# Kernel optimization log

Hardware: AMD Instinct MI355X
Metric: run time of the kernel (lower is better)

## Reference

```python
import jax, jax.numpy as jnp
import numpy as np

# DeepSeek V4 MLA sparse attention dims
T = 512            # query tokens
H = 64             # attention heads (SUPPORTED_HEAD_COUNTS)
KV_LORA = 512      # kv_lora_rank (value dim = latent nope part)
ROPE = 64          # qk_rope_head_dim
D = KV_LORA + ROPE # 576 = head_dim (matches alignment=576 in cache spec)
N_KV = 8192        # cached compressed-KV tokens
TOPK = 1024        # top-k selected tokens per query
SCALE = 1.0 / np.sqrt(D).astype(np.float32)


def setup_inputs() -> dict:
    key = jax.random.key(0)
    k1, k2, k3, k4 = jax.random.split(key, 4)
    q = jax.random.normal(k1, (T, H, D), dtype=jnp.float32)
    kv = jax.random.normal(k2, (N_KV, D), dtype=jnp.float32)   # compressed KV latent cache (1 kv head)
    topk_idx = jax.random.randint(k3, (T, TOPK), 0, N_KV, dtype=jnp.int32)
    sink = jax.random.normal(k4, (H,), dtype=jnp.float32)       # per-head attention sink logit
    return {"q": q, "kv": kv, "topk_idx": topk_idx, "sink": sink}


def reference(q, kv, topk_idx, sink):
    # Sparse MLA: each query token attends only to its top-k latent cache slots.
    valid = topk_idx >= 0                       # invalid slots marked negative
    idx = jnp.maximum(topk_idx, 0)
    g = kv[idx]                                  # [T, K, D] gathered latents
    # scores over gathered subset: [T, H, K]
    scores = jnp.einsum('thd,tkd->thk', q, g) * SCALE
    scores = jnp.where(valid[:, None, :], scores, -jnp.inf)
    # sink-aware softmax: sink acts as an extra logit with zero value
    m = jnp.maximum(jnp.max(scores, axis=-1), sink[None, :])   # [T, H]
    p = jnp.exp(scores - m[..., None])                          # [T, H, K]
    denom = jnp.sum(p, axis=-1) + jnp.exp(sink[None, :] - m)    # [T, H]
    # value = nope part (first KV_LORA dims) of latent -> output [T, H, KV_LORA]
    out = jnp.einsum('thk,tkv->thv', p, g[..., :KV_LORA]) / denom[..., None]
    return out
```

## Files before the change

### kernel.cpp

```cpp
#include <hip/hip_runtime.h>
#include <hip/hip_bf16.h>

#define T_TOK 512
#define NH    64
#define HD    576
#define DVAL  512
#define NKV   8192
#define TOPK  1024
#define KT    32
#define NITER (TOPK / KT)
#define KSTEPS (HD / 32)
#define SCALE 0.041666666666666664f
#define LOG2E 1.4426950408889634f
#define QSCL  (SCALE * LOG2E)
#define MFIX  8.0f
#define MB    (MFIX * LOG2E)

typedef __attribute__((ext_vector_type(4))) float f32x4;
typedef __attribute__((ext_vector_type(8))) _Float16 half8;
typedef __attribute__((ext_vector_type(4))) unsigned short us4;
typedef __attribute__((ext_vector_type(8))) unsigned short us8;
typedef __attribute__((ext_vector_type(4))) int i32x4;

__device__ __forceinline__ unsigned short f2h(float x) {
    _Float16 h = (_Float16)x;
    return __builtin_bit_cast(unsigned short, h);
}

__device__ __forceinline__ float fexp2(float x) {
#if __has_builtin(__builtin_amdgcn_exp2f)
    return __builtin_amdgcn_exp2f(x);
#else
    return __expf(x * 0.6931471805599453f);
#endif
}

template<int CTRL>
__device__ __forceinline__ float dppmv(float x) {
    int r = __builtin_amdgcn_update_dpp(0, __builtin_bit_cast(int, x), CTRL, 0xF, 0xF, true);
    return __builtin_bit_cast(float, r);
}
__device__ __forceinline__ float red16sum(float x) {
    x += dppmv<0xB1>(x);
    x += dppmv<0x4E>(x);
    x += dppmv<0x141>(x);
    x += dppmv<0x140>(x);
    return x;
}

#define TICK_BARRIER() do {                                   \
    asm volatile("s_waitcnt lgkmcnt(0)" ::: "memory");        \
    __builtin_amdgcn_s_barrier();                             \
    asm volatile("" ::: "memory");                            \
} while (0)

__global__ void cvt_kv_f16(const float* __restrict__ kv, unsigned short* __restrict__ kvb) {
    int i = blockIdx.x * 256 + threadIdx.x;
    const f32x4* src = (const f32x4*)kv + (size_t)i * 2;
    f32x4 a = src[0];
    f32x4 b = src[1];
    us8 w;
    w[0]=f2h(a[0]); w[1]=f2h(a[1]); w[2]=f2h(a[2]); w[3]=f2h(a[3]);
    w[4]=f2h(b[0]); w[5]=f2h(b[1]); w[6]=f2h(b[2]); w[7]=f2h(b[3]);
    ((us8*)kvb)[i] = w;
}

#define G_LD  584
#define P_LD  40
#define GT_IDX(row,key) (((((row) << 5) | (key))) ^ ((((row) >> 2) & 7) << 3))

struct StageRegs { us8 v[4]; us4 rope; };

__device__ __forceinline__ void stage_load(
    const unsigned short* __restrict__ kvb, const int* __restrict__ tkrow,
    int it, int w8, int kg, int lm, int quad, int l16, StageRegs& R)
{
    const int* ip = tkrow + it * KT + kg * 4;
    i32x4 r4 = *(const i32x4*)ip;
    int d0 = w8 * 64 + lm * 8;
    #pragma unroll
    for (int j = 0; j < 4; j++) {
        int r = r4[j] < 0 ? 0 : r4[j];
        R.v[j] = *(const us8*)(kvb + (size_t)r * HD + d0);
    }
    int kr = tkrow[it * KT + w8 * 4 + quad];
    if (kr < 0) kr = 0;
    R.rope = *(const us4*)(kvb + (size_t)kr * HD + 512 + l16 * 4);
}

__device__ __forceinline__ void stage_write(
    int w8, int kg, int lm, int quad, int l16, const StageRegs& R,
    unsigned short (*gp)[G_LD], unsigned short* gtp)
{
    int d0 = w8 * 64 + lm * 8;
    #pragma unroll
    for (int j = 0; j < 4; j++)
        *(us8*)&gp[kg * 4 + j][d0] = R.v[j];
    #pragma unroll
    for (int e = 0; e < 8; e++) {
        us4 wv;
        wv[0] = R.v[0][e]; wv[1] = R.v[1][e]; wv[2] = R.v[2][e]; wv[3] = R.v[3][e];
        *(us4*)&gtp[GT_IDX(d0 + e, kg * 4)] = wv;
    }
    *(us4*)&gp[w8 * 4 + quad][512 + l16 * 4] = R.rope;
}

__device__ __forceinline__ void pv_tick(
    int tau, const unsigned short* __restrict__ kvb, const int* __restrict__ tkrow,
    int w8, int kg, int lm, int quad, int l16, int col0,
    StageRegs& Lset, StageRegs& Wset,
    unsigned short (*g2p)[G_LD], unsigned short* gtp,
    const unsigned short (*pb)[P_LD],
    f32x4 (&acc)[4][4])
{
    if (tau + 2 < NITER)
        stage_load(kvb, tkrow, tau + 2, w8, kg, lm, quad, l16, Lset);

    half8 pa[4];
    #pragma unroll
    for (int mt = 0; mt < 4; mt++)
        pa[mt] = *(const half8*)&pb[mt * 16 + l16][quad * 8];

    __builtin_amdgcn_s_setprio(1);
    #pragma unroll
    for (int nt = 0; nt < 4; nt++) {
        half8 vb = *(const half8*)&gtp[GT_IDX(col0 + nt * 16 + l16, quad * 8)];
        #pragma unroll
        for (int mt = 0; mt < 4; mt++)
            acc[mt][nt] = __builtin_amdgcn_mfma_f32_16x16x32_f16(pa[mt], vb, acc[mt][nt], 0, 0, 0);
    }
    __builtin_amdgcn_s_setprio(0);

    asm volatile("s_waitcnt lgkmcnt(0)" ::: "memory");
    if (tau + 1 < NITER)
        stage_write(w8, kg, lm, quad, l16, Wset, g2p, gtp);
}

__global__ __launch_bounds__(768, 3) void mla_sparse_kernel(
    const float* __restrict__ q, const int* __restrict__ topk,
    const float* __restrict__ sink, const unsigned short* __restrict__ kvb,
    float* __restrict__ out)
{
    __shared__ unsigned short g2[2][KT][G_LD];
    __shared__ unsigned short gtb[2][DVAL * KT];
    __shared__ unsigned short pbuf[2][NH][P_LD];
    __shared__ float lrunL[NH];

    const int t    = blockIdx.x;
    const int tid  = threadIdx.x;
    const int lane = tid & 63;
    const int quad = lane >> 4;
    const int l16  = lane & 15;
    const int wave = __builtin_amdgcn_readfirstlane(tid >> 6);
    const int* tkrow = topk + (size_t)t * TOPK;

    if (wave < 4) {
        const int w  = wave;
        const int qo = quad * 8;
        half8 qf[KSTEPS];
        {
            const float* qrow = q + ((size_t)t * NH + (w * 16 + l16)) * HD;
            #pragma unroll
            for (int ks = 0; ks < KSTEPS; ks++) {
                int d0 = ks * 32 + qo;
                f32x4 a = *(const f32x4*)(qrow + d0);
                f32x4 b = *(const f32x4*)(qrow + d0 + 4);
                half8 h;
                h[0]=(_Float16)(a[0]*QSCL); h[1]=(_Float16)(a[1]*QSCL);
                h[2]=(_Float16)(a[2]*QSCL); h[3]=(_Float16)(a[3]*QSCL);
                h[4]=(_Float16)(b[0]*QSCL); h[5]=(_Float16)(b[1]*QSCL);
                h[6]=(_Float16)(b[2]*QSCL); h[7]=(_Float16)(b[3]*QSCL);
                qf[ks] = h;
            }
        }
        unsigned mb0 = 0, mb1 = 0;
        #pragma unroll 4
        for (int kk = 0; kk < NITER; kk++) {
            mb0 |= (tkrow[kk * KT + l16]      < 0) ? (1u << kk) : 0u;
            mb1 |= (tkrow[kk * KT + 16 + l16] < 0) ? (1u << kk) : 0u;
        }
        f32x4 sk = *(const f32x4*)(sink + w * 16 + quad * 4);
        float l_part[4];
        #pragma unroll
        for (int r = 0; r < 4; r++)
            l_part[r] = (l16 == 0) ? fexp2(sk[r] * LOG2E - MB) : 0.0f;
        const int hb = w * 16 + quad * 4;

        __syncthreads();

        for (int k = 0; k <= NITER; k++) {
            if (k < NITER) {
                const int par = k & 1;
                const unsigned short (*gp)[G_LD] = g2[par];
                f32x4 zero = {0.f, 0.f, 0.f, 0.f};
                f32x4 mbase = {-MB, -MB, -MB, -MB};
                f32x4 s0a = mbase, s0b = zero, s1a = mbase, s1b = zero;
                __builtin_amdgcn_s_setprio(1);
                #pragma unroll
                for (int ks = 0; ks < KSTEPS; ks += 2) {
                    half8 b0 = *(const half8*)&gp[l16][ks * 32 + qo];
                    half8 b1 = *(const half8*)&gp[16 + l16][ks * 32 + qo];
                    s0a = __builtin_amdgcn_mfma_f32_16x16x32_f16(qf[ks], b0, s0a, 0, 0, 0);
                    s1a = __builtin_amdgcn_mfma_f32_16x16x32_f16(qf[ks], b1, s1a, 0, 0, 0);
                    half8 c0 = *(const half8*)&gp[l16][ks * 32 + 32 + qo];
                    half8 c1 = *(const half8*)&gp[16 + l16][ks * 32 + 32 + qo];
                    s0b = __builtin_amdgcn_mfma_f32_16x16x32_f16(qf[ks+1], c0, s0b, 0, 0, 0);
                    s1b = __builtin_amdgcn_mfma_f32_16x16x32_f16(qf[ks+1], c1, s1b, 0, 0, 0);
                }
                __builtin_amdgcn_s_setprio(0);
                f32x4 s0 = s0a + s0b, s1 = s1a + s1b;
                const bool bad0 = (mb0 >> k) & 1;
                const bool bad1 = (mb1 >> k) & 1;
                const float NEG = -__builtin_inff();
                #pragma unroll
                for (int r = 0; r < 4; r++) {
                    float v0 = bad0 ? NEG : s0[r];
                    float v1 = bad1 ? NEG : s1[r];
                    float p0 = fexp2(v0);
                    float p1 = fexp2(v1);
                    l_part[r] += p0 + p1;
                    pbuf[par][hb + r][l16]      = f2h(p0);
                    pbuf[par][hb + r][16 + l16] = f2h(p1);
                }
            }
            TICK_BARRIER();
        }
        #pragma unroll
        for (int r = 0; r < 4; r++) l_part[r] = red16sum(l_part[r]);
        if (l16 == 0) {
            f32x4 l4; l4[0]=l_part[0]; l4[1]=l_part[1]; l4[2]=l_part[2]; l4[3]=l_part[3];
            *(f32x4*)&lrunL[hb] = l4;
        }
        __syncthreads();
    } else {
        const int w8   = wave - 4;
        const int col0 = w8 * 64;
        const int kg   = lane >> 3;
        const int lm   = lane & 7;
        f32x4 acc[4][4];
        f32x4 zero = {0.f, 0.f, 0.f, 0.f};
        #pragma unroll
        for (int mt = 0; mt < 4; mt++)
            #pragma unroll
            for (int nt = 0; nt < 4; nt++) acc[mt][nt] = zero;

        StageRegs A, B;
        stage_load(kvb, tkrow, 0, w8, kg, lm, quad, l16, A);
        stage_write(w8, kg, lm, quad, l16, A, g2[0], gtb[0]);
        stage_load(kvb, tkrow, 1, w8, kg, lm, quad, l16, B);
        __syncthreads();

        stage_load(kvb, tkrow, 2, w8, kg, lm, quad, l16, A);
        stage_write(w8, kg, lm, quad, l16, B, g2[1], gtb[1]);
        TICK_BARRIER();

        for (int k = 1; k < NITER; k += 2) {
            pv_tick(k, kvb, tkrow, w8, kg, lm, quad, l16, col0,
                    B, A, g2[0], gtb[0], pbuf[0], acc);
            TICK_BARRIER();
            pv_tick(k + 1, kvb, tkrow, w8, kg, lm, quad, l16, col0,
                    A, B, g2[1], gtb[1], pbuf[1], acc);
            TICK_BARRIER();
        }
        __syncthreads();

        #pragma unroll
        for (int mt = 0; mt < 4; mt++) {
            f32x4 lv = *(const f32x4*)&lrunL[mt * 16 + quad * 4];
            f32x4 li;
            li[0] = 1.0f / lv[0]; li[1] = 1.0f / lv[1];
            li[2] = 1.0f / lv[2]; li[3] = 1.0f / lv[3];
            #pragma unroll
            for (int nt = 0; nt < 4; nt++) {
                int vcol = col0 + nt * 16 + l16;
                f32x4 r = acc[mt][nt] * li;
                #pragma unroll
                for (int rr = 0; rr < 4; rr++) {
                    int head = mt * 16 + quad * 4 + rr;
                    out[((size_t)t * NH + head) * DVAL + vcol] = r[rr];
                }
            }
        }
    }
}

extern "C" void kernel_launch(void* const* d_in, const int* in_sizes, int n_in,
                              void* d_out, int out_size, void* d_ws, size_t ws_size,
                              hipStream_t stream) {
    const float* q    = (const float*)d_in[0];
    const float* kv   = (const float*)d_in[1];
    const int*   topk = (const int*)d_in[2];
    const float* sink = (const float*)d_in[3];
    float* out = (float*)d_out;
    unsigned short* kvb = (unsigned short*)d_ws;

    cvt_kv_f16<<<NKV * HD / (256 * 8), 256, 0, stream>>>(kv, kvb);
    mla_sparse_kernel<<<T_TOK, 768, 0, stream>>>(q, topk, sink, kvb, out);
}
```

Baseline: 255.5 us.

## Load rope slice directly from global in score waves instead of LDS staging

The PV producer waves no longer stage the 64-wide rope part of each gathered KV row into shared memory. Instead the score waves fetch their rope fragments straight from global memory each iteration and feed them to the final MFMAs. This shrinks the LDS row stride from 584 to 520 and drops the precomputed invalid-index bitmasks, which are now derived from the per-iteration index loads. The trade-off is added global-load latency on the score path, which sits on the critical QK path with no prefetch.

```diff
diff --git a/kernel.cpp b/kernel.cpp
--- a/kernel.cpp
+++ b/kernel.cpp
@@ -9,7 +9,7 @@
 #define TOPK  1024
 #define KT    32
 #define NITER (TOPK / KT)
-#define KSTEPS (HD / 32)
+#define KSTEPS_L 16
 #define SCALE 0.041666666666666664f
 #define LOG2E 1.4426950408889634f
 #define QSCL  (SCALE * LOG2E)
@@ -65,15 +65,15 @@
     ((us8*)kvb)[i] = w;
 }
 
-#define G_LD  584
+#define G_LD  520
 #define P_LD  40
 #define GT_IDX(row,key) (((((row) << 5) | (key))) ^ ((((row) >> 2) & 7) << 3))
 
-struct StageRegs { us8 v[4]; us4 rope; };
+struct StageRegs { us8 v[4]; };
 
 __device__ __forceinline__ void stage_load(
     const unsigned short* __restrict__ kvb, const int* __restrict__ tkrow,
-    int it, int w8, int kg, int lm, int quad, int l16, StageRegs& R)
+    int it, int w8, int kg, int lm, StageRegs& R)
 {
     const int* ip = tkrow + it * KT + kg * 4;
     i32x4 r4 = *(const i32x4*)ip;
@@ -83,13 +83,10 @@
         int r = r4[j] < 0 ? 0 : r4[j];
         R.v[j] = *(const us8*)(kvb + (size_t)r * HD + d0);
     }
-    int kr = tkrow[it * KT + w8 * 4 + quad];
-    if (kr < 0) kr = 0;
-    R.rope = *(const us4*)(kvb + (size_t)kr * HD + 512 + l16 * 4);
 }
 
 __device__ __forceinline__ void stage_write(
-    int w8, int kg, int lm, int quad, int l16, const StageRegs& R,
+    int w8, int kg, int lm, const StageRegs& R,
     unsigned short (*gp)[G_LD], unsigned short* gtp)
 {
     int d0 = w8 * 64 + lm * 8;
@@ -102,7 +99,6 @@
         wv[0] = R.v[0][e]; wv[1] = R.v[1][e]; wv[2] = R.v[2][e]; wv[3] = R.v[3][e];
         *(us4*)&gtp[GT_IDX(d0 + e, kg * 4)] = wv;
     }
-    *(us4*)&gp[w8 * 4 + quad][512 + l16 * 4] = R.rope;
 }
 
 __device__ __forceinline__ void pv_tick(
@@ -114,7 +110,7 @@
     f32x4 (&acc)[4][4])
 {
     if (tau + 2 < NITER)
-        stage_load(kvb, tkrow, tau + 2, w8, kg, lm, quad, l16, Lset);
+        stage_load(kvb, tkrow, tau + 2, w8, kg, lm, Lset);
 
     half8 pa[4];
     #pragma unroll
@@ -133,7 +129,7 @@
 
     asm volatile("s_waitcnt lgkmcnt(0)" ::: "memory");
     if (tau + 1 < NITER)
-        stage_write(w8, kg, lm, quad, l16, Wset, g2p, gtp);
+        stage_write(w8, kg, lm, Wset, g2p, gtp);
 }
 
 __global__ __launch_bounds__(768, 3) void mla_sparse_kernel(
@@ -157,11 +153,11 @@
     if (wave < 4) {
         const int w  = wave;
         const int qo = quad * 8;
-        half8 qf[KSTEPS];
+        half8 qf[18];
         {
             const float* qrow = q + ((size_t)t * NH + (w * 16 + l16)) * HD;
             #pragma unroll
-            for (int ks = 0; ks < KSTEPS; ks++) {
+            for (int ks = 0; ks < 18; ks++) {
                 int d0 = ks * 32 + qo;
                 f32x4 a = *(const f32x4*)(qrow + d0);
                 f32x4 b = *(const f32x4*)(qrow + d0 + 4);
@@ -173,12 +169,6 @@
                 qf[ks] = h;
             }
         }
-        unsigned mb0 = 0, mb1 = 0;
-        #pragma unroll 4
-        for (int kk = 0; kk < NITER; kk++) {
-            mb0 |= (tkrow[kk * KT + l16]      < 0) ? (1u << kk) : 0u;
-            mb1 |= (tkrow[kk * KT + 16 + l16] < 0) ? (1u << kk) : 0u;
-        }
         f32x4 sk = *(const f32x4*)(sink + w * 16 + quad * 4);
         float l_part[4];
         #pragma unroll
@@ -192,12 +182,23 @@
             if (k < NITER) {
                 const int par = k & 1;
                 const unsigned short (*gp)[G_LD] = g2[par];
+                int raw0 = tkrow[k * KT + l16];
+                int raw1 = tkrow[k * KT + 16 + l16];
+                int ra = raw0 < 0 ? 0 : raw0;
+                int rb = raw1 < 0 ? 0 : raw1;
+                const unsigned short* rpA = kvb + (size_t)ra * HD + 512 + qo;
+                const unsigned short* rpB = kvb + (size_t)rb * HD + 512 + qo;
+                half8 r0a = *(const half8*)(rpA);
+                half8 r0b = *(const half8*)(rpB);
+                half8 r1a = *(const half8*)(rpA + 32);
+                half8 r1b = *(const half8*)(rpB + 32);
+
                 f32x4 zero = {0.f, 0.f, 0.f, 0.f};
                 f32x4 mbase = {-MB, -MB, -MB, -MB};
                 f32x4 s0a = mbase, s0b = zero, s1a = mbase, s1b = zero;
                 __builtin_amdgcn_s_setprio(1);
                 #pragma unroll
-                for (int ks = 0; ks < KSTEPS; ks += 2) {
+                for (int ks = 0; ks < KSTEPS_L; ks += 2) {
                     half8 b0 = *(const half8*)&gp[l16][ks * 32 + qo];
                     half8 b1 = *(const half8*)&gp[16 + l16][ks * 32 + qo];
                     s0a = __builtin_amdgcn_mfma_f32_16x16x32_f16(qf[ks], b0, s0a, 0, 0, 0);
@@ -207,10 +208,14 @@
                     s0b = __builtin_amdgcn_mfma_f32_16x16x32_f16(qf[ks+1], c0, s0b, 0, 0, 0);
                     s1b = __builtin_amdgcn_mfma_f32_16x16x32_f16(qf[ks+1], c1, s1b, 0, 0, 0);
                 }
+                s0a = __builtin_amdgcn_mfma_f32_16x16x32_f16(qf[16], r0a, s0a, 0, 0, 0);
+                s1a = __builtin_amdgcn_mfma_f32_16x16x32_f16(qf[16], r0b, s1a, 0, 0, 0);
+                s0b = __builtin_amdgcn_mfma_f32_16x16x32_f16(qf[17], r1a, s0b, 0, 0, 0);
+                s1b = __builtin_amdgcn_mfma_f32_16x16x32_f16(qf[17], r1b, s1b, 0, 0, 0);
                 __builtin_amdgcn_s_setprio(0);
                 f32x4 s0 = s0a + s0b, s1 = s1a + s1b;
-                const bool bad0 = (mb0 >> k) & 1;
-                const bool bad1 = (mb1 >> k) & 1;
+                const bool bad0 = raw0 < 0;
+                const bool bad1 = raw1 < 0;
                 const float NEG = -__builtin_inff();
                 #pragma unroll
                 for (int r = 0; r < 4; r++) {
@@ -245,13 +250,13 @@
             for (int nt = 0; nt < 4; nt++) acc[mt][nt] = zero;
 
         StageRegs A, B;
-        stage_load(kvb, tkrow, 0, w8, kg, lm, quad, l16, A);
-        stage_write(w8, kg, lm, quad, l16, A, g2[0], gtb[0]);
-        stage_load(kvb, tkrow, 1, w8, kg, lm, quad, l16, B);
+        stage_load(kvb, tkrow, 0, w8, kg, lm, A);
+        stage_write(w8, kg, lm, A, g2[0], gtb[0]);
+        stage_load(kvb, tkrow, 1, w8, kg, lm, B);
         __syncthreads();
 
-        stage_load(kvb, tkrow, 2, w8, kg, lm, quad, l16, A);
-        stage_write(w8, kg, lm, quad, l16, B, g2[1], gtb[1]);
+        stage_load(kvb, tkrow, 2, w8, kg, lm, A);
+        stage_write(w8, kg, lm, B, g2[1], gtb[1]);
         TICK_BARRIER();
 
         for (int k = 1; k < NITER; k += 2) {
```

New measurement: 263.1 us. 1.03x slower.

## Load gathered KV rows directly into LDS via global_load_lds with swizzled layout

Applied to the files above, without the earlier changes.

The row-major gathered KV tile and its rope part are now fetched with direct global-to-LDS loads (global_load_lds) into a new XOR-swizzled 512-wide layout plus a separate rope buffer, instead of going through registers and ds_write. The QK waves index the swizzled layout. The register path stays only for the transposed copy used by PV, and explicit vmcnt waits order the asynchronous loads before the barriers. This is meant to cut VGPR traffic and LDS write instructions on the producer waves, but it loads the nope part twice from global memory and depends on hand-counted vmcnt values being correct.

```diff
diff --git a/kernel.cpp b/kernel.cpp
--- a/kernel.cpp
+++ b/kernel.cpp
@@ -9,7 +9,6 @@
 #define TOPK  1024
 #define KT    32
 #define NITER (TOPK / KT)
-#define KSTEPS (HD / 32)
 #define SCALE 0.041666666666666664f
 #define LOG2E 1.4426950408889634f
 #define QSCL  (SCALE * LOG2E)
@@ -53,6 +52,16 @@
     __builtin_amdgcn_s_barrier();                             \
     asm volatile("" ::: "memory");                            \
 } while (0)
+
+#if __has_builtin(__builtin_amdgcn_global_load_lds)
+#define HAVE_GLOAD 1
+#define GLOAD16(src, ldsbase)                                              \
+    __builtin_amdgcn_global_load_lds(                                      \
+        (const __attribute__((address_space(1))) void*)(src),              \
+        (__attribute__((address_space(3))) void*)(ldsbase), 16, 0, 0)
+#else
+#define HAVE_GLOAD 0
+#endif
 
 __global__ void cvt_kv_f16(const float* __restrict__ kv, unsigned short* __restrict__ kvb) {
     int i = blockIdx.x * 256 + threadIdx.x;
@@ -65,15 +74,51 @@
     ((us8*)kvb)[i] = w;
 }
 
-#define G_LD  584
 #define P_LD  40
 #define GT_IDX(row,key) (((((row) << 5) | (key))) ^ ((((row) >> 2) & 7) << 3))
 
-struct StageRegs { us8 v[4]; us4 rope; };
+struct StageRegs { us8 v[4]; };
+
+__device__ __forceinline__ void stage_gload(
+    const unsigned short* __restrict__ kvb, const int* __restrict__ tkrow,
+    int it, int w8, int lane, unsigned short* g2d, unsigned short* roped)
+{
+#if HAVE_GLOAD
+    #pragma unroll
+    for (int j = 0; j < 4; j++) {
+        int key = w8 * 4 + j;
+        int row = tkrow[it * KT + key]; row = row < 0 ? 0 : row;
+        int chunk = lane ^ (key & 7);
+        GLOAD16(kvb + (size_t)row * HD + chunk * 8, g2d + key * 512);
+    }
+    if (w8 < 4) {
+        int key = w8 * 8 + (lane >> 3);
+        int row = tkrow[it * KT + key]; row = row < 0 ? 0 : row;
+        int chunk = (lane & 7) ^ (key & 7);
+        GLOAD16(kvb + (size_t)row * HD + 512 + chunk * 8, roped + w8 * 512);
+    }
+#else
+    #pragma unroll
+    for (int j = 0; j < 4; j++) {
+        int key = w8 * 4 + j;
+        int row = tkrow[it * KT + key]; row = row < 0 ? 0 : row;
+        int chunk = lane ^ (key & 7);
+        *(us8*)&g2d[key * 512 + lane * 8] =
+            *(const us8*)(kvb + (size_t)row * HD + chunk * 8);
+    }
+    if (w8 < 4) {
+        int key = w8 * 8 + (lane >> 3);
+        int row = tkrow[it * KT + key]; row = row < 0 ? 0 : row;
+        int chunk = (lane & 7) ^ (key & 7);
+        *(us8*)&roped[w8 * 512 + lane * 8] =
+            *(const us8*)(kvb + (size_t)row * HD + 512 + chunk * 8);
+    }
+#endif
+}
 
 __device__ __forceinline__ void stage_load(
     const unsigned short* __restrict__ kvb, const int* __restrict__ tkrow,
-    int it, int w8, int kg, int lm, int quad, int l16, StageRegs& R)
+    int it, int w8, int kg, int lm, StageRegs& R)
 {
     const int* ip = tkrow + it * KT + kg * 4;
     i32x4 r4 = *(const i32x4*)ip;
@@ -83,38 +128,34 @@
         int r = r4[j] < 0 ? 0 : r4[j];
         R.v[j] = *(const us8*)(kvb + (size_t)r * HD + d0);
     }
-    int kr = tkrow[it * KT + w8 * 4 + quad];
-    if (kr < 0) kr = 0;
-    R.rope = *(const us4*)(kvb + (size_t)kr * HD + 512 + l16 * 4);
-}
-
-__device__ __forceinline__ void stage_write(
-    int w8, int kg, int lm, int quad, int l16, const StageRegs& R,
-    unsigned short (*gp)[G_LD], unsigned short* gtp)
+}
+
+__device__ __forceinline__ void stage_write_gt(
+    int w8, int kg, int lm, const StageRegs& R, unsigned short* gtp)
 {
     int d0 = w8 * 64 + lm * 8;
-    #pragma unroll
-    for (int j = 0; j < 4; j++)
-        *(us8*)&gp[kg * 4 + j][d0] = R.v[j];
     #pragma unroll
     for (int e = 0; e < 8; e++) {
         us4 wv;
         wv[0] = R.v[0][e]; wv[1] = R.v[1][e]; wv[2] = R.v[2][e]; wv[3] = R.v[3][e];
         *(us4*)&gtp[GT_IDX(d0 + e, kg * 4)] = wv;
     }
-    *(us4*)&gp[w8 * 4 + quad][512 + l16 * 4] = R.rope;
 }
 
 __device__ __forceinline__ void pv_tick(
     int tau, const unsigned short* __restrict__ kvb, const int* __restrict__ tkrow,
-    int w8, int kg, int lm, int quad, int l16, int col0,
+    int w8, int kg, int lm, int quad, int l16, int lane, int col0,
     StageRegs& Lset, StageRegs& Wset,
-    unsigned short (*g2p)[G_LD], unsigned short* gtp,
+    unsigned short* g2d_next, unsigned short* roped_next, unsigned short* gtp,
     const unsigned short (*pb)[P_LD],
     f32x4 (&acc)[4][4])
 {
-    if (tau + 2 < NITER)
-        stage_load(kvb, tkrow, tau + 2, w8, kg, lm, quad, l16, Lset);
+    const bool do_next  = (tau + 1 < NITER);
+    const bool do_load2 = (tau + 2 < NITER);
+    if (do_next)
+        stage_gload(kvb, tkrow, tau + 1, w8, lane, g2d_next, roped_next);
+    if (do_load2)
+        stage_load(kvb, tkrow, tau + 2, w8, kg, lm, Lset);
 
     half8 pa[4];
     #pragma unroll
@@ -132,8 +173,11 @@
     __builtin_amdgcn_s_setprio(0);
 
     asm volatile("s_waitcnt lgkmcnt(0)" ::: "memory");
-    if (tau + 1 < NITER)
-        stage_write(w8, kg, lm, quad, l16, Wset, g2p, gtp);
+    if (do_next) {
+        stage_write_gt(w8, kg, lm, Wset, gtp);
+        if (do_load2) asm volatile("s_waitcnt vmcnt(4)" ::: "memory");
+        else          asm volatile("s_waitcnt vmcnt(0)" ::: "memory");
+    }
 }
 
 __global__ __launch_bounds__(768, 3) void mla_sparse_kernel(
@@ -141,27 +185,28 @@
     const float* __restrict__ sink, const unsigned short* __restrict__ kvb,
     float* __restrict__ out)
 {
-    __shared__ unsigned short g2[2][KT][G_LD];
+    __shared__ unsigned short g2s[2][KT * 512];
+    __shared__ unsigned short ropes[2][KT * 64];
     __shared__ unsigned short gtb[2][DVAL * KT];
     __shared__ unsigned short pbuf[2][NH][P_LD];
     __shared__ float lrunL[NH];
 
-    const int t    = blockIdx.x;
     const int tid  = threadIdx.x;
     const int lane = tid & 63;
     const int quad = lane >> 4;
     const int l16  = lane & 15;
     const int wave = __builtin_amdgcn_readfirstlane(tid >> 6);
+    const int t    = blockIdx.x;
     const int* tkrow = topk + (size_t)t * TOPK;
 
     if (wave < 4) {
         const int w  = wave;
         const int qo = quad * 8;
-        half8 qf[KSTEPS];
+        half8 qf[18];
         {
             const float* qrow = q + ((size_t)t * NH + (w * 16 + l16)) * HD;
             #pragma unroll
-            for (int ks = 0; ks < KSTEPS; ks++) {
+            for (int ks = 0; ks < 18; ks++) {
                 int d0 = ks * 32 + qo;
                 f32x4 a = *(const f32x4*)(qrow + d0);
                 f32x4 b = *(const f32x4*)(qrow + d0 + 4);
@@ -179,6 +224,11 @@
             mb0 |= (tkrow[kk * KT + l16]      < 0) ? (1u << kk) : 0u;
             mb1 |= (tkrow[kk * KT + 16 + l16] < 0) ? (1u << kk) : 0u;
         }
+        const int k7    = l16 & 7;
+        const int sidx0 = l16 * 512 + ((quad ^ k7) << 3);
+        const int sidx1 = l16 * 512 + (((4 + quad) ^ k7) << 3);
+        const int ridx0 = l16 * 64 + ((quad ^ k7) << 3);
+        const int ridx1 = l16 * 64 + (((4 + quad) ^ k7) << 3);
         f32x4 sk = *(const f32x4*)(sink + w * 16 + quad * 4);
         float l_part[4];
         #pragma unroll
@@ -191,21 +241,33 @@
         for (int k = 0; k <= NITER; k++) {
             if (k < NITER) {
                 const int par = k & 1;
-                const unsigned short (*gp)[G_LD] = g2[par];
+                const unsigned short* gp = g2s[par];
+                const unsigned short* rp = ropes[par];
                 f32x4 zero = {0.f, 0.f, 0.f, 0.f};
                 f32x4 mbase = {-MB, -MB, -MB, -MB};
                 f32x4 s0a = mbase, s0b = zero, s1a = mbase, s1b = zero;
                 __builtin_amdgcn_s_setprio(1);
                 #pragma unroll
-                for (int ks = 0; ks < KSTEPS; ks += 2) {
-                    half8 b0 = *(const half8*)&gp[l16][ks * 32 + qo];
-                    half8 b1 = *(const half8*)&gp[16 + l16][ks * 32 + qo];
+                for (int ks = 0; ks < 16; ks += 2) {
+                    int o = (ks >> 1) * 64;
+                    half8 b0 = *(const half8*)&gp[sidx0 + o];
+                    half8 b1 = *(const half8*)&gp[sidx0 + 8192 + o];
                     s0a = __builtin_amdgcn_mfma_f32_16x16x32_f16(qf[ks], b0, s0a, 0, 0, 0);
                     s1a = __builtin_amdgcn_mfma_f32_16x16x32_f16(qf[ks], b1, s1a, 0, 0, 0);
-                    half8 c0 = *(const half8*)&gp[l16][ks * 32 + 32 + qo];
-                    half8 c1 = *(const half8*)&gp[16 + l16][ks * 32 + 32 + qo];
+                    half8 c0 = *(const half8*)&gp[sidx1 + o];
+                    half8 c1 = *(const half8*)&gp[sidx1 + 8192 + o];
                     s0b = __builtin_amdgcn_mfma_f32_16x16x32_f16(qf[ks+1], c0, s0b, 0, 0, 0);
                     s1b = __builtin_amdgcn_mfma_f32_16x16x32_f16(qf[ks+1], c1, s1b, 0, 0, 0);
+                }
+                {
+                    half8 r0 = *(const half8*)&rp[ridx0];
+                    half8 r1 = *(const half8*)&rp[ridx0 + 1024];
+                    s0a = __builtin_amdgcn_mfma_f32_16x16x32_f16(qf[16], r0, s0a, 0, 0, 0);
+                    s1a = __builtin_amdgcn_mfma_f32_16x16x32_f16(qf[16], r1, s1a, 0, 0, 0);
+                    half8 r2 = *(const half8*)&rp[ridx1];
+                    half8 r3 = *(const half8*)&rp[ridx1 + 1024];
+                    s0b = __builtin_amdgcn_mfma_f32_16x16x32_f16(qf[17], r2, s0b, 0, 0, 0);
+                    s1b = __builtin_amdgcn_mfma_f32_16x16x32_f16(qf[17], r3, s1b, 0, 0, 0);
                 }
                 __builtin_amdgcn_s_setprio(0);
                 f32x4 s0 = s0a + s0b, s1 = s1a + s1b;
@@ -245,21 +307,26 @@
             for (int nt = 0; nt < 4; nt++) acc[mt][nt] = zero;
 
         StageRegs A, B;
-        stage_load(kvb, tkrow, 0, w8, kg, lm, quad, l16, A);
-        stage_write(w8, kg, lm, quad, l16, A, g2[0], gtb[0]);
-        stage_load(kvb, tkrow, 1, w8, kg, lm, quad, l16, B);
+        stage_gload(kvb, tkrow, 0, w8, lane, g2s[0], ropes[0]);
+        stage_load(kvb, tkrow, 0, w8, kg, lm, A);
+        stage_write_gt(w8, kg, lm, A, gtb[0]);
+        stage_load(kvb, tkrow, 1, w8, kg, lm, B);
+        asm volatile("s_waitcnt vmcnt(4)" ::: "memory");
         __syncthreads();
 
-        stage_load(kvb, tkrow, 2, w8, kg, lm, quad, l16, A);
-        stage_write(w8, kg, lm, quad, l16, B, g2[1], gtb[1]);
+        stage_gload(kvb, tkrow, 1, w8, lane, g2s[1], ropes[1]);
+        stage_load(kvb, tkrow, 2, w8, kg, lm, A);
+        asm volatile("s_waitcnt lgkmcnt(0)" ::: "memory");
+        stage_write_gt(w8, kg, lm, B, gtb[1]);
+        asm volatile("s_waitcnt vmcnt(4)" ::: "memory");
         TICK_BARRIER();
 
         for (int k = 1; k < NITER; k += 2) {
-            pv_tick(k, kvb, tkrow, w8, kg, lm, quad, l16, col0,
-                    B, A, g2[0], gtb[0], pbuf[0], acc);
+            pv_tick(k, kvb, tkrow, w8, kg, lm, quad, l16, lane, col0,
+                    B, A, g2s[0], ropes[0], gtb[0], pbuf[0], acc);
             TICK_BARRIER();
-            pv_tick(k + 1, kvb, tkrow, w8, kg, lm, quad, l16, col0,
-                    A, B, g2[1], gtb[1], pbuf[1], acc);
+            pv_tick(k + 1, kvb, tkrow, w8, kg, lm, quad, l16, lane, col0,
+                    A, B, g2s[1], ropes[1], gtb[1], pbuf[1], acc);
             TICK_BARRIER();
         }
         __syncthreads();
```

Measured after the change: 258.0 us. About the same (+1.0%).

## Use ds_read_b64_tr_b16 transpose reads instead of separate transposed LDS copy

Applied to the files above, without the earlier changes.

Replaces the dual LDS layout (row-major gathered KV plus a separately written transposed copy for the PV matmul) with a single subtiled layout of 4-key groups. The PV waves now read V operands with the hardware transposing LDS load ds_read_b64_tr_b16, and the QK waves index into the new subtile layout. This removes the per-element scatter of the transposed buffer and halves LDS footprint, at the cost of inline asm, a full lgkmcnt wait before the MFMAs, and new bank-conflict behavior from the subtile stride.

```diff
diff --git a/kernel.cpp b/kernel.cpp
--- a/kernel.cpp
+++ b/kernel.cpp
@@ -9,12 +9,14 @@
 #define TOPK  1024
 #define KT    32
 #define NITER (TOPK / KT)
-#define KSTEPS (HD / 32)
+#define KSTEPS 18
 #define SCALE 0.041666666666666664f
 #define LOG2E 1.4426950408889634f
 #define QSCL  (SCALE * LOG2E)
 #define MFIX  8.0f
 #define MB    (MFIX * LOG2E)
+#define SKG   2312
+#define P_LD  36
 
 typedef __attribute__((ext_vector_type(4))) float f32x4;
 typedef __attribute__((ext_vector_type(8))) _Float16 half8;
@@ -65,10 +67,6 @@
     ((us8*)kvb)[i] = w;
 }
 
-#define G_LD  584
-#define P_LD  40
-#define GT_IDX(row,key) (((((row) << 5) | (key))) ^ ((((row) >> 2) & 7) << 3))
-
 struct StageRegs { us8 v[4]; us4 rope; };
 
 __device__ __forceinline__ void stage_load(
@@ -88,28 +86,24 @@
     R.rope = *(const us4*)(kvb + (size_t)kr * HD + 512 + l16 * 4);
 }
 
-__device__ __forceinline__ void stage_write(
+__device__ __forceinline__ void stage_write_sub(
     int w8, int kg, int lm, int quad, int l16, const StageRegs& R,
-    unsigned short (*gp)[G_LD], unsigned short* gtp)
+    unsigned short* g2d)
 {
-    int d0 = w8 * 64 + lm * 8;
+    int chunk = w8 * 4 + (lm >> 1);
+    int off   = (lm & 1) * 8;
+    int base  = kg * SKG + chunk * 64 + off;
     #pragma unroll
     for (int j = 0; j < 4; j++)
-        *(us8*)&gp[kg * 4 + j][d0] = R.v[j];
-    #pragma unroll
-    for (int e = 0; e < 8; e++) {
-        us4 wv;
-        wv[0] = R.v[0][e]; wv[1] = R.v[1][e]; wv[2] = R.v[2][e]; wv[3] = R.v[3][e];
-        *(us4*)&gtp[GT_IDX(d0 + e, kg * 4)] = wv;
-    }
-    *(us4*)&gp[w8 * 4 + quad][512 + l16 * 4] = R.rope;
+        *(us8*)&g2d[base + j * 16] = R.v[j];
+    *(us4*)&g2d[w8 * SKG + (32 + (l16 >> 2)) * 64 + quad * 16 + (l16 & 3) * 4] = R.rope;
 }
 
 __device__ __forceinline__ void pv_tick(
     int tau, const unsigned short* __restrict__ kvb, const int* __restrict__ tkrow,
     int w8, int kg, int lm, int quad, int l16, int col0,
     StageRegs& Lset, StageRegs& Wset,
-    unsigned short (*g2p)[G_LD], unsigned short* gtp,
+    unsigned short* g2_w, const unsigned short* g2_r,
     const unsigned short (*pb)[P_LD],
     f32x4 (&acc)[4][4])
 {
@@ -121,19 +115,33 @@
     for (int mt = 0; mt < 4; mt++)
         pa[mt] = *(const half8*)&pb[mt * 16 + l16][quad * 8];
 
+    us4 t0[4], t1[4];
+    const unsigned gbase = (unsigned)(size_t)g2_r;
+    #pragma unroll
+    for (int nt = 0; nt < 4; nt++) {
+        unsigned a0 = gbase + 2u * ((quad * 2 + 0) * SKG + (w8 * 4 + nt) * 64) + 8u * l16;
+        unsigned a1 = gbase + 2u * ((quad * 2 + 1) * SKG + (w8 * 4 + nt) * 64) + 8u * l16;
+        asm volatile("ds_read_b64_tr_b16 %0, %1" : "=v"(t0[nt]) : "v"(a0));
+        asm volatile("ds_read_b64_tr_b16 %0, %1" : "=v"(t1[nt]) : "v"(a1));
+    }
+    asm volatile("s_waitcnt lgkmcnt(0)" ::: "memory");
+    __builtin_amdgcn_sched_barrier(0);
+
     __builtin_amdgcn_s_setprio(1);
     #pragma unroll
     for (int nt = 0; nt < 4; nt++) {
-        half8 vb = *(const half8*)&gtp[GT_IDX(col0 + nt * 16 + l16, quad * 8)];
+        us8 wv;
+        wv[0]=t0[nt][0]; wv[1]=t0[nt][1]; wv[2]=t0[nt][2]; wv[3]=t0[nt][3];
+        wv[4]=t1[nt][0]; wv[5]=t1[nt][1]; wv[6]=t1[nt][2]; wv[7]=t1[nt][3];
+        half8 vb = __builtin_bit_cast(half8, wv);
         #pragma unroll
         for (int mt = 0; mt < 4; mt++)
             acc[mt][nt] = __builtin_amdgcn_mfma_f32_16x16x32_f16(pa[mt], vb, acc[mt][nt], 0, 0, 0);
     }
     __builtin_amdgcn_s_setprio(0);
 
-    asm volatile("s_waitcnt lgkmcnt(0)" ::: "memory");
     if (tau + 1 < NITER)
-        stage_write(w8, kg, lm, quad, l16, Wset, g2p, gtp);
+        stage_write_sub(w8, kg, lm, quad, l16, Wset, g2_w);
 }
 
 __global__ __launch_bounds__(768, 3) void mla_sparse_kernel(
@@ -141,17 +149,16 @@
     const float* __restrict__ sink, const unsigned short* __restrict__ kvb,
     float* __restrict__ out)
 {
-    __shared__ unsigned short g2[2][KT][G_LD];
-    __shared__ unsigned short gtb[2][DVAL * KT];
+    __shared__ unsigned short g2sub[2][8 * SKG];
     __shared__ unsigned short pbuf[2][NH][P_LD];
     __shared__ float lrunL[NH];
 
-    const int t    = blockIdx.x;
     const int tid  = threadIdx.x;
     const int lane = tid & 63;
     const int quad = lane >> 4;
     const int l16  = lane & 15;
     const int wave = __builtin_amdgcn_readfirstlane(tid >> 6);
+    const int t    = blockIdx.x;
     const int* tkrow = topk + (size_t)t * TOPK;
 
     if (wave < 4) {
@@ -179,6 +186,8 @@
             mb0 |= (tkrow[kk * KT + l16]      < 0) ? (1u << kk) : 0u;
             mb1 |= (tkrow[kk * KT + 16 + l16] < 0) ? (1u << kk) : 0u;
         }
+        const int baseA = (l16 >> 2) * SKG + (l16 & 3) * 16 + (quad >> 1) * 64 + (quad & 1) * 8;
+        const int baseB = baseA + 4 * SKG;
         f32x4 sk = *(const f32x4*)(sink + w * 16 + quad * 4);
         float l_part[4];
         #pragma unroll
@@ -191,19 +200,19 @@
         for (int k = 0; k <= NITER; k++) {
             if (k < NITER) {
                 const int par = k & 1;
-                const unsigned short (*gp)[G_LD] = g2[par];
+                const unsigned short* gp = g2sub[par];
                 f32x4 zero = {0.f, 0.f, 0.f, 0.f};
                 f32x4 mbase = {-MB, -MB, -MB, -MB};
                 f32x4 s0a = mbase, s0b = zero, s1a = mbase, s1b = zero;
                 __builtin_amdgcn_s_setprio(1);
                 #pragma unroll
                 for (int ks = 0; ks < KSTEPS; ks += 2) {
-                    half8 b0 = *(const half8*)&gp[l16][ks * 32 + qo];
-                    half8 b1 = *(const half8*)&gp[16 + l16][ks * 32 + qo];
+                    half8 b0 = *(const half8*)&gp[baseA + ks * 128];
+                    half8 b1 = *(const half8*)&gp[baseB + ks * 128];
                     s0a = __builtin_amdgcn_mfma_f32_16x16x32_f16(qf[ks], b0, s0a, 0, 0, 0);
                     s1a = __builtin_amdgcn_mfma_f32_16x16x32_f16(qf[ks], b1, s1a, 0, 0, 0);
-                    half8 c0 = *(const half8*)&gp[l16][ks * 32 + 32 + qo];
-                    half8 c1 = *(const half8*)&gp[16 + l16][ks * 32 + 32 + qo];
+                    half8 c0 = *(const half8*)&gp[baseA + (ks + 1) * 128];
+                    half8 c1 = *(const half8*)&gp[baseB + (ks + 1) * 128];
                     s0b = __builtin_amdgcn_mfma_f32_16x16x32_f16(qf[ks+1], c0, s0b, 0, 0, 0);
                     s1b = __builtin_amdgcn_mfma_f32_16x16x32_f16(qf[ks+1], c1, s1b, 0, 0, 0);
                 }
@@ -246,20 +255,20 @@
 
         StageRegs A, B;
         stage_load(kvb, tkrow, 0, w8, kg, lm, quad, l16, A);
-        stage_write(w8, kg, lm, quad, l16, A, g2[0], gtb[0]);
+        stage_write_sub(w8, kg, lm, quad, l16, A, g2sub[0]);
         stage_load(kvb, tkrow, 1, w8, kg, lm, quad, l16, B);
         __syncthreads();
 
         stage_load(kvb, tkrow, 2, w8, kg, lm, quad, l16, A);
-        stage_write(w8, kg, lm, quad, l16, B, g2[1], gtb[1]);
+        stage_write_sub(w8, kg, lm, quad, l16, B, g2sub[1]);
         TICK_BARRIER();
 
         for (int k = 1; k < NITER; k += 2) {
             pv_tick(k, kvb, tkrow, w8, kg, lm, quad, l16, col0,
-                    B, A, g2[0], gtb[0], pbuf[0], acc);
+                    B, A, g2sub[0], g2sub[0], pbuf[0], acc);
             TICK_BARRIER();
             pv_tick(k + 1, kvb, tkrow, w8, kg, lm, quad, l16, col0,
-                    A, B, g2[1], gtb[1], pbuf[1], acc);
+                    A, B, g2sub[1], g2sub[1], pbuf[1], acc);
             TICK_BARRIER();
         }
         __syncthreads();
```

New measurement: 307.4 us. 20.3% more time.
